# Kernel optimization log

Measured on AMD Instinct MI355X. Metric: run time of the kernel, lower is better.

Reference implementation:

```python
import jax, jax.numpy as jnp
import numpy as np

NUM_NODES = 100000
EMBED_DIM = 64
NUM_LAYERS = 3
NUM_EDGES = 3200000


def setup_inputs() -> dict:
    key = jax.random.key(0)
    k1, k2 = jax.random.split(key)
    # xavier_uniform for [N, D]: bound = sqrt(6/(N+D))
    bound = float(np.sqrt(6.0 / (NUM_NODES + EMBED_DIM)))
    emb = jax.random.uniform(k1, (NUM_NODES, EMBED_DIM), dtype=jnp.float32,
                             minval=-bound, maxval=bound)
    edge_index = jax.random.randint(k2, (2, NUM_EDGES), 0, NUM_NODES, dtype=jnp.int64)
    return {"emb": emb, "edge_index": edge_index}


def reference(emb, edge_index):
    # LightGCN: xs = [x0, LGConv(x0), LGConv^2(x0), ...]; output = mean(xs)
    # LGConv (PyG, add_self_loops=False): out[i] = sum_{(j,i) in E} x[j] / sqrt(d_j * d_i)
    n = emb.shape[0]
    row, col = edge_index[0], edge_index[1]  # row = source j, col = target i
    ones = jnp.ones(row.shape[0], dtype=emb.dtype)
    deg = jax.ops.segment_sum(ones, col, num_segments=n)  # in-degree per gcn_norm
    dinv = jnp.where(deg > 0, jax.lax.rsqrt(jnp.where(deg > 0, deg, 1.0)), 0.0)
    norm = dinv[row] * dinv[col]  # [E]

    x = emb
    acc = emb
    for _ in range(NUM_LAYERS):
        msgs = x[row] * norm[:, None]                      # gather + normalize [E, D]
        x = jax.ops.segment_sum(msgs, col, num_segments=n)  # scatter-add [N, D]
        acc = acc + x
    return acc / (NUM_LAYERS + 1)
```

## Files before the change

kernel.cpp:

```cpp
#include <hip/hip_runtime.h>
#include <hip/hip_bf16.h>
#include <stdint.h>


#define N_NODES 100000
#define N_EDGES 3200000
#define DIM 64

#define NB 196
#define BSH 9
#define BNODES 512
#define CAP 20480

#define CHUNK 8192
#define NBLK1 ((N_EDGES + CHUNK - 1) / CHUNK)

__device__ __forceinline__ float bl(unsigned u) { return __uint_as_float(u << 16); }
__device__ __forceinline__ float bh(unsigned u) { return __uint_as_float(u & 0xffff0000u); }

__global__ __launch_bounds__(256) void k_bucket(const int* __restrict__ ei,
                                                int* __restrict__ gcursor,
                                                int* __restrict__ staging) {
    __shared__ int stage[CHUNK];
    __shared__ unsigned char sbkt[CHUNK];
    __shared__ int bcnt[NB];
    __shared__ int boff[NB];
    __shared__ int bstart[NB];
    __shared__ int gbase[NB];
    __shared__ int wt[4];

    int t = threadIdx.x;
    int e0 = blockIdx.x * CHUNK;
    int nblk = min(CHUNK, N_EDGES - e0);
    int nvec = nblk >> 2;

    const int4* col4 = (const int4*)(ei + N_EDGES + e0);
    const int4* row4 = (const int4*)(ei + e0);

    for (int i = t; i < NB; i += 256) { bcnt[i] = 0; boff[i] = 0; }
    __syncthreads();

    for (int i = t; i < nvec; i += 256) {
        int4 c = col4[i];
        atomicAdd(&bcnt[c.x >> BSH], 1);
        atomicAdd(&bcnt[c.y >> BSH], 1);
        atomicAdd(&bcnt[c.z >> BSH], 1);
        atomicAdd(&bcnt[c.w >> BSH], 1);
    }
    __syncthreads();

    {
        int v = (t < NB) ? bcnt[t] : 0;
        int lane = t & 63, w = t >> 6;
        int s = v;
#pragma unroll
        for (int off = 1; off < 64; off <<= 1) {
            int u = __shfl_up(s, off);
            if (lane >= off) s += u;
        }
        if (lane == 63) wt[w] = s;
        __syncthreads();
        int wo = 0;
        for (int ww = 0; ww < w; ww++) wo += wt[ww];
        if (t < NB) {
            bstart[t] = s - v + wo;
            gbase[t] = (v > 0) ? atomicAdd(&gcursor[t], v) : 0;
        }
    }
    __syncthreads();

    for (int i = t; i < nvec; i += 256) {
        int4 c = col4[i];
        int4 r = row4[i];
        int b0 = c.x >> BSH, b1 = c.y >> BSH, b2 = c.z >> BSH, b3 = c.w >> BSH;
        int p0 = bstart[b0] + atomicAdd(&boff[b0], 1);
        int p1 = bstart[b1] + atomicAdd(&boff[b1], 1);
        int p2 = bstart[b2] + atomicAdd(&boff[b2], 1);
        int p3 = bstart[b3] + atomicAdd(&boff[b3], 1);
        stage[p0] = (r.x << BSH) | (c.x & (BNODES - 1)); sbkt[p0] = (unsigned char)b0;
        stage[p1] = (r.y << BSH) | (c.y & (BNODES - 1)); sbkt[p1] = (unsigned char)b1;
        stage[p2] = (r.z << BSH) | (c.z & (BNODES - 1)); sbkt[p2] = (unsigned char)b2;
        stage[p3] = (r.w << BSH) | (c.w & (BNODES - 1)); sbkt[p3] = (unsigned char)b3;
    }
    __syncthreads();

    for (int i = t; i < nblk; i += 256) {
        int e = stage[i];
        int b = sbkt[i];
        staging[(size_t)b * CAP + gbase[b] + (i - bstart[b])] = e;
    }
}

__global__ void k_bstart(const int* __restrict__ gcursor, int* __restrict__ bucketStart) {
    __shared__ int wt[4];
    int t = threadIdx.x;
    int v = (t < NB) ? gcursor[t] : 0;
    int lane = t & 63, w = t >> 6;
    int s = v;
#pragma unroll
    for (int off = 1; off < 64; off <<= 1) {
        int u = __shfl_up(s, off);
        if (lane >= off) s += u;
    }
    if (lane == 63) wt[w] = s;
    __syncthreads();
    int wo = 0;
    for (int ww = 0; ww < w; ww++) wo += wt[ww];
    if (t < NB) bucketStart[t] = s - v + wo;
}

__global__ __launch_bounds__(256) void k_build(const int* __restrict__ gcursor,
                                               const int* __restrict__ bucketStart,
                                               const int* __restrict__ staging,
                                               int* __restrict__ deg,
                                               int* __restrict__ base,
                                               float* __restrict__ dinv,
                                               int* __restrict__ csrc) {
    __shared__ int ldeg[BNODES];
    __shared__ int lcur[BNODES];
    __shared__ int wt[4];

    int b = blockIdx.x;
    int t = threadIdx.x;
    int n0 = b << BSH;
    int nloc = min(BNODES, N_NODES - n0);
    int cnt = gcursor[b];
    const int* st = staging + (size_t)b * CAP;

    ldeg[t] = 0; ldeg[t + 256] = 0;
    __syncthreads();

    for (int i = t; i < cnt; i += 256) {
        atomicAdd(&ldeg[st[i] & (BNODES - 1)], 1);
    }
    __syncthreads();

    int a0 = ldeg[2 * t], a1 = ldeg[2 * t + 1];
    int s = a0 + a1;
    int lane = t & 63, w = t >> 6;
    int ss = s;
#pragma unroll
    for (int off = 1; off < 64; off <<= 1) {
        int u = __shfl_up(ss, off);
        if (lane >= off) ss += u;
    }
    if (lane == 63) wt[w] = ss;
    __syncthreads();
    int wo = 0;
    for (int ww = 0; ww < w; ww++) wo += wt[ww];
    int excl = ss - s + wo;

    int gb = bucketStart[b] + excl;
    int n = n0 + 2 * t;
    lcur[2 * t] = gb;
    lcur[2 * t + 1] = gb + a0;
    if (2 * t < nloc) {
        deg[n] = a0;
        base[n] = gb;
        dinv[n] = (a0 > 0) ? rsqrtf((float)a0) : 0.0f;
    }
    if (2 * t + 1 < nloc) {
        deg[n + 1] = a1;
        base[n + 1] = gb + a0;
        dinv[n + 1] = (a1 > 0) ? rsqrtf((float)a1) : 0.0f;
    }
    __syncthreads();

    for (int i = t; i < cnt; i += 256) {
        int e = st[i];
        int p = atomicAdd(&lcur[e & (BNODES - 1)], 1);
        csrc[p] = e >> BSH;
    }
}

__global__ void k_z0(const float* __restrict__ emb, const float* __restrict__ dinv,
                     __hip_bfloat16* __restrict__ z) {
    int i = blockIdx.x * blockDim.x + threadIdx.x;
    if (i >= (N_NODES * DIM) / 4) return;
    float di = dinv[(i * 4) >> 6];
    const float4 v = ((const float4*)emb)[i];
    union { ushort h[4]; uint2 u; } pk;
    __hip_bfloat16 b0 = __float2bfloat16(v.x * di);
    __hip_bfloat16 b1 = __float2bfloat16(v.y * di);
    __hip_bfloat16 b2 = __float2bfloat16(v.z * di);
    __hip_bfloat16 b3 = __float2bfloat16(v.w * di);
    pk.h[0] = *(ushort*)&b0; pk.h[1] = *(ushort*)&b1;
    pk.h[2] = *(ushort*)&b2; pk.h[3] = *(ushort*)&b3;
    ((uint2*)z)[i] = pk.u;
}

__global__ __launch_bounds__(256) void k_spmv(
    const int* __restrict__ base, const int* __restrict__ deg,
    const int* __restrict__ csrc, const __hip_bfloat16* __restrict__ z,
    const float* __restrict__ dinv, __hip_bfloat16* __restrict__ znext,
    const float* __restrict__ emb, float* __restrict__ acc_out, int mode) {
    int wave = (blockIdx.x * blockDim.x + threadIdx.x) >> 6;
    int lane = threadIdx.x & 63;
    if (wave >= N_NODES) return;
    int g = lane >> 3;
    int l = lane & 7;

    int start = base[wave];
    int cnt = deg[wave];
    int last = start + max(cnt - 1, 0);

    float acc[8] = {0, 0, 0, 0, 0, 0, 0, 0};

#define ACCUM(U)                                   \
    do {                                           \
        acc[0] += bl((U).x); acc[1] += bh((U).x);  \
        acc[2] += bl((U).y); acc[3] += bh((U).y);  \
        acc[4] += bl((U).z); acc[5] += bh((U).z);  \
        acc[6] += bl((U).w); acc[7] += bh((U).w);  \
    } while (0)

    for (int pos = 0; pos < cnt; pos += 32) {
        int e = pos + g;
        int i0 = start + e;
        int j0 = min(i0, last);
        int j1 = min(i0 + 8, last);
        int j2 = min(i0 + 16, last);
        int j3 = min(i0 + 24, last);
        int s0 = csrc[j0];
        int s1 = csrc[j1];
        int s2 = csrc[j2];
        int s3 = csrc[j3];
        if (e >= cnt)      s0 = N_NODES;
        if (e + 8 >= cnt)  s1 = N_NODES;
        if (e + 16 >= cnt) s2 = N_NODES;
        if (e + 24 >= cnt) s3 = N_NODES;
        uint4 v0 = *((const uint4*)(z + ((size_t)s0 << 6)) + l);
        uint4 v1 = *((const uint4*)(z + ((size_t)s1 << 6)) + l);
        uint4 v2 = *((const uint4*)(z + ((size_t)s2 << 6)) + l);
        uint4 v3 = *((const uint4*)(z + ((size_t)s3 << 6)) + l);
        ACCUM(v0); ACCUM(v1); ACCUM(v2); ACCUM(v3);
    }
#undef ACCUM

#pragma unroll
    for (int j = 0; j < 8; j++) {
        acc[j] += __shfl_xor(acc[j], 8);
        acc[j] += __shfl_xor(acc[j], 16);
        acc[j] += __shfl_xor(acc[j], 32);
    }

    if (lane < 8) {
        float di = dinv[wave];
        size_t o = (size_t)wave * DIM + lane * 8;
        float xo[8];
#pragma unroll
        for (int j = 0; j < 8; j++) xo[j] = acc[j] * di;

        float4 o0, o1;
        if (mode == 0) {
            float4 e0 = ((const float4*)(emb + o))[0];
            float4 e1 = ((const float4*)(emb + o))[1];
            o0 = make_float4(e0.x + xo[0], e0.y + xo[1], e0.z + xo[2], e0.w + xo[3]);
            o1 = make_float4(e1.x + xo[4], e1.y + xo[5], e1.z + xo[6], e1.w + xo[7]);
        } else if (mode == 1) {
            float4 a0 = ((const float4*)(acc_out + o))[0];
            float4 a1 = ((const float4*)(acc_out + o))[1];
            o0 = make_float4(a0.x + xo[0], a0.y + xo[1], a0.z + xo[2], a0.w + xo[3]);
            o1 = make_float4(a1.x + xo[4], a1.y + xo[5], a1.z + xo[6], a1.w + xo[7]);
        } else {
            float4 a0 = ((const float4*)(acc_out + o))[0];
            float4 a1 = ((const float4*)(acc_out + o))[1];
            o0 = make_float4((a0.x + xo[0]) * 0.25f, (a0.y + xo[1]) * 0.25f,
                             (a0.z + xo[2]) * 0.25f, (a0.w + xo[3]) * 0.25f);
            o1 = make_float4((a1.x + xo[4]) * 0.25f, (a1.y + xo[5]) * 0.25f,
                             (a1.z + xo[6]) * 0.25f, (a1.w + xo[7]) * 0.25f);
        }
        ((float4*)(acc_out + o))[0] = o0;
        ((float4*)(acc_out + o))[1] = o1;

        if (mode != 2) {
            union { ushort h[8]; uint4 u; } pk;
#pragma unroll
            for (int j = 0; j < 8; j++) {
                __hip_bfloat16 b = __float2bfloat16(xo[j] * di);
                pk.h[j] = *(ushort*)&b;
            }
            *((uint4*)(znext + o)) = pk.u;
        }
    }
}

extern "C" void kernel_launch(void* const* d_in, const int* in_sizes, int n_in,
                              void* d_out, int out_size, void* d_ws, size_t ws_size,
                              hipStream_t stream) {
    const float* emb = (const float*)d_in[0];
    const int* ei = (const int*)d_in[1];
    float* out = (float*)d_out;

    char* ws = (char*)d_ws;
    size_t off = 0;
    auto alloc = [&](size_t bytes) -> void* {
        void* p = ws + off;
        off += (bytes + 511) & ~(size_t)511;
        return p;
    };
    int* deg = (int*)alloc((size_t)N_NODES * 4);
    float* dinv = (float*)alloc((size_t)N_NODES * 4);
    int* base = (int*)alloc((size_t)N_NODES * 4);
    int* gcursor = (int*)alloc(NB * 4);
    int* bucketStart = (int*)alloc(NB * 4);
    int* csrc = (int*)alloc((size_t)N_EDGES * 4);
    size_t zbytes = (size_t)(N_NODES + 1) * DIM * 2;
    size_t stbytes = (size_t)NB * CAP * 4;
    char* transient = (char*)alloc(stbytes > zbytes ? stbytes : zbytes);
    int* staging = (int*)transient;
    __hip_bfloat16* zA = (__hip_bfloat16*)transient;
    __hip_bfloat16* zB = (__hip_bfloat16*)alloc(zbytes);

    hipMemsetAsync(gcursor, 0, NB * 4, stream);

    k_bucket<<<NBLK1, 256, 0, stream>>>(ei, gcursor, staging);
    k_bstart<<<1, 256, 0, stream>>>(gcursor, bucketStart);
    k_build<<<NB, 256, 0, stream>>>(gcursor, bucketStart, staging, deg, base, dinv, csrc);
    k_z0<<<(N_NODES * DIM / 4 + 255) / 256, 256, 0, stream>>>(emb, dinv, zA);
    hipMemsetAsync(zA + (size_t)N_NODES * DIM, 0, DIM * 2, stream);
    hipMemsetAsync(zB + (size_t)N_NODES * DIM, 0, DIM * 2, stream);

    int spmvBlocks = (N_NODES + 3) / 4;
    k_spmv<<<spmvBlocks, 256, 0, stream>>>(base, deg, csrc, zA, dinv, zB, emb, out, 0);
    k_spmv<<<spmvBlocks, 256, 0, stream>>>(base, deg, csrc, zB, dinv, zA, emb, out, 1);
    k_spmv<<<spmvBlocks, 256, 0, stream>>>(base, deg, csrc, zA, dinv, zB, emb, out, 2);
}
```

Before: 337.7 us.

## Switch gathered features to fp16 with packed half2 accumulation and fold memsets

The normalized feature tables are stored as fp16 instead of bf16, and the SpMV gather now accumulates with packed half2 adds instead of eight fp32 accumulators. Neighbor loads use an exact group count with a remainder path instead of clamped indices. The two sentinel-row memsets are folded into the z0 kernel, and the bucketing chunk size is halved. Accumulating in fp16 reduces ALU work and register use, but it risks precision loss and overflow on sums over high-degree nodes.

```diff
diff --git a/kernel.cpp b/kernel.cpp
--- a/kernel.cpp
+++ b/kernel.cpp
@@ -1,5 +1,6 @@
 #include <hip/hip_runtime.h>
 #include <hip/hip_bf16.h>
+#include <hip/hip_fp16.h>
 #include <stdint.h>
 
 
@@ -12,11 +13,8 @@
 #define BNODES 512
 #define CAP 20480
 
-#define CHUNK 8192
+#define CHUNK 4096
 #define NBLK1 ((N_EDGES + CHUNK - 1) / CHUNK)
-
-__device__ __forceinline__ float bl(unsigned u) { return __uint_as_float(u << 16); }
-__device__ __forceinline__ float bh(unsigned u) { return __uint_as_float(u & 0xffff0000u); }
 
 __global__ __launch_bounds__(256) void k_bucket(const int* __restrict__ ei,
                                                 int* __restrict__ gcursor,
@@ -174,25 +172,31 @@
 }
 
 __global__ void k_z0(const float* __restrict__ emb, const float* __restrict__ dinv,
-                     __hip_bfloat16* __restrict__ z) {
+                     __half* __restrict__ zA, __half* __restrict__ zB) {
+    const int total = (N_NODES * DIM) / 4;
     int i = blockIdx.x * blockDim.x + threadIdx.x;
-    if (i >= (N_NODES * DIM) / 4) return;
+    if (i >= total) {
+        int r = i - total;
+        if (r < 16) ((uint2*)(zA + (size_t)N_NODES * DIM))[r] = make_uint2(0, 0);
+        else if (r < 32) ((uint2*)(zB + (size_t)N_NODES * DIM))[r - 16] = make_uint2(0, 0);
+        return;
+    }
     float di = dinv[(i * 4) >> 6];
     const float4 v = ((const float4*)emb)[i];
     union { ushort h[4]; uint2 u; } pk;
-    __hip_bfloat16 b0 = __float2bfloat16(v.x * di);
-    __hip_bfloat16 b1 = __float2bfloat16(v.y * di);
-    __hip_bfloat16 b2 = __float2bfloat16(v.z * di);
-    __hip_bfloat16 b3 = __float2bfloat16(v.w * di);
-    pk.h[0] = *(ushort*)&b0; pk.h[1] = *(ushort*)&b1;
-    pk.h[2] = *(ushort*)&b2; pk.h[3] = *(ushort*)&b3;
-    ((uint2*)z)[i] = pk.u;
+    __half h0 = __float2half(v.x * di);
+    __half h1 = __float2half(v.y * di);
+    __half h2 = __float2half(v.z * di);
+    __half h3 = __float2half(v.w * di);
+    pk.h[0] = *(ushort*)&h0; pk.h[1] = *(ushort*)&h1;
+    pk.h[2] = *(ushort*)&h2; pk.h[3] = *(ushort*)&h3;
+    ((uint2*)zA)[i] = pk.u;
 }
 
 __global__ __launch_bounds__(256) void k_spmv(
     const int* __restrict__ base, const int* __restrict__ deg,
-    const int* __restrict__ csrc, const __hip_bfloat16* __restrict__ z,
-    const float* __restrict__ dinv, __hip_bfloat16* __restrict__ znext,
+    const int* __restrict__ csrc, const __half* __restrict__ z,
+    const float* __restrict__ dinv, __half* __restrict__ znext,
     const float* __restrict__ emb, float* __restrict__ acc_out, int mode) {
     int wave = (blockIdx.x * blockDim.x + threadIdx.x) >> 6;
     int lane = threadIdx.x & 63;
@@ -202,54 +206,62 @@
 
     int start = base[wave];
     int cnt = deg[wave];
-    int last = start + max(cnt - 1, 0);
-
-    float acc[8] = {0, 0, 0, 0, 0, 0, 0, 0};
-
-#define ACCUM(U)                                   \
-    do {                                           \
-        acc[0] += bl((U).x); acc[1] += bh((U).x);  \
-        acc[2] += bl((U).y); acc[3] += bh((U).y);  \
-        acc[4] += bl((U).z); acc[5] += bh((U).z);  \
-        acc[6] += bl((U).w); acc[7] += bh((U).w);  \
+    float di = dinv[wave];
+    int ng = (cnt + 7) >> 3;
+
+    __half2 hz = __float2half2_rn(0.0f);
+    __half2 hacc0 = hz, hacc1 = hz, hacc2 = hz, hacc3 = hz;
+
+#define GLOAD(KK, SVAR)                              \
+    int e##SVAR = (KK) * 8 + g;                      \
+    int SVAR = csrc[start + e##SVAR];                \
+    SVAR = (e##SVAR < cnt) ? SVAR : N_NODES;
+
+#define GACC(SVAR)                                                        \
+    do {                                                                  \
+        uint4 v = *((const uint4*)(z + ((size_t)SVAR << 6)) + l);         \
+        const __half2* hv = (const __half2*)&v;                           \
+        hacc0 = __hadd2(hacc0, hv[0]);                                    \
+        hacc1 = __hadd2(hacc1, hv[1]);                                    \
+        hacc2 = __hadd2(hacc2, hv[2]);                                    \
+        hacc3 = __hadd2(hacc3, hv[3]);                                    \
     } while (0)
 
-    for (int pos = 0; pos < cnt; pos += 32) {
-        int e = pos + g;
-        int i0 = start + e;
-        int j0 = min(i0, last);
-        int j1 = min(i0 + 8, last);
-        int j2 = min(i0 + 16, last);
-        int j3 = min(i0 + 24, last);
-        int s0 = csrc[j0];
-        int s1 = csrc[j1];
-        int s2 = csrc[j2];
-        int s3 = csrc[j3];
-        if (e >= cnt)      s0 = N_NODES;
-        if (e + 8 >= cnt)  s1 = N_NODES;
-        if (e + 16 >= cnt) s2 = N_NODES;
-        if (e + 24 >= cnt) s3 = N_NODES;
-        uint4 v0 = *((const uint4*)(z + ((size_t)s0 << 6)) + l);
-        uint4 v1 = *((const uint4*)(z + ((size_t)s1 << 6)) + l);
-        uint4 v2 = *((const uint4*)(z + ((size_t)s2 << 6)) + l);
-        uint4 v3 = *((const uint4*)(z + ((size_t)s3 << 6)) + l);
-        ACCUM(v0); ACCUM(v1); ACCUM(v2); ACCUM(v3);
-    }
-#undef ACCUM
-
-#pragma unroll
-    for (int j = 0; j < 8; j++) {
-        acc[j] += __shfl_xor(acc[j], 8);
-        acc[j] += __shfl_xor(acc[j], 16);
-        acc[j] += __shfl_xor(acc[j], 32);
+    int k = 0;
+    for (; k + 4 <= ng; k += 4) {
+        GLOAD(k + 0, s0); GLOAD(k + 1, s1); GLOAD(k + 2, s2); GLOAD(k + 3, s3);
+        GACC(s0); GACC(s1); GACC(s2); GACC(s3);
+    }
+    int rem = ng - k;
+    if (rem > 0) {
+        GLOAD(k + 0, t0);
+        if (rem > 1) { GLOAD(k + 1, t1);
+            if (rem > 2) { GLOAD(k + 2, t2); GACC(t0); GACC(t1); GACC(t2); }
+            else { GACC(t0); GACC(t1); }
+        } else { GACC(t0); }
+    }
+#undef GLOAD
+#undef GACC
+
+#pragma unroll
+    for (int off = 8; off <= 32; off <<= 1) {
+        int b0 = __shfl_xor(*(int*)&hacc0, off);
+        int b1 = __shfl_xor(*(int*)&hacc1, off);
+        int b2 = __shfl_xor(*(int*)&hacc2, off);
+        int b3 = __shfl_xor(*(int*)&hacc3, off);
+        hacc0 = __hadd2(hacc0, *(__half2*)&b0);
+        hacc1 = __hadd2(hacc1, *(__half2*)&b1);
+        hacc2 = __hadd2(hacc2, *(__half2*)&b2);
+        hacc3 = __hadd2(hacc3, *(__half2*)&b3);
     }
 
     if (lane < 8) {
-        float di = dinv[wave];
         size_t o = (size_t)wave * DIM + lane * 8;
         float xo[8];
-#pragma unroll
-        for (int j = 0; j < 8; j++) xo[j] = acc[j] * di;
+        xo[0] = __low2float(hacc0) * di; xo[1] = __high2float(hacc0) * di;
+        xo[2] = __low2float(hacc1) * di; xo[3] = __high2float(hacc1) * di;
+        xo[4] = __low2float(hacc2) * di; xo[5] = __high2float(hacc2) * di;
+        xo[6] = __low2float(hacc3) * di; xo[7] = __high2float(hacc3) * di;
 
         float4 o0, o1;
         if (mode == 0) {
@@ -277,8 +289,8 @@
             union { ushort h[8]; uint4 u; } pk;
 #pragma unroll
             for (int j = 0; j < 8; j++) {
-                __hip_bfloat16 b = __float2bfloat16(xo[j] * di);
-                pk.h[j] = *(ushort*)&b;
+                __half hh = __float2half(xo[j] * di);
+                pk.h[j] = *(ushort*)&hh;
             }
             *((uint4*)(znext + o)) = pk.u;
         }
@@ -304,22 +316,20 @@
     int* base = (int*)alloc((size_t)N_NODES * 4);
     int* gcursor = (int*)alloc(NB * 4);
     int* bucketStart = (int*)alloc(NB * 4);
-    int* csrc = (int*)alloc((size_t)N_EDGES * 4);
+    int* csrc = (int*)alloc(((size_t)N_EDGES + 64) * 4);
     size_t zbytes = (size_t)(N_NODES + 1) * DIM * 2;
     size_t stbytes = (size_t)NB * CAP * 4;
     char* transient = (char*)alloc(stbytes > zbytes ? stbytes : zbytes);
     int* staging = (int*)transient;
-    __hip_bfloat16* zA = (__hip_bfloat16*)transient;
-    __hip_bfloat16* zB = (__hip_bfloat16*)alloc(zbytes);
+    __half* zA = (__half*)transient;
+    __half* zB = (__half*)alloc(zbytes);
 
     hipMemsetAsync(gcursor, 0, NB * 4, stream);
 
     k_bucket<<<NBLK1, 256, 0, stream>>>(ei, gcursor, staging);
     k_bstart<<<1, 256, 0, stream>>>(gcursor, bucketStart);
     k_build<<<NB, 256, 0, stream>>>(gcursor, bucketStart, staging, deg, base, dinv, csrc);
-    k_z0<<<(N_NODES * DIM / 4 + 255) / 256, 256, 0, stream>>>(emb, dinv, zA);
-    hipMemsetAsync(zA + (size_t)N_NODES * DIM, 0, DIM * 2, stream);
-    hipMemsetAsync(zB + (size_t)N_NODES * DIM, 0, DIM * 2, stream);
+    k_z0<<<(N_NODES * DIM / 4) / 256 + 1, 256, 0, stream>>>(emb, dinv, zA, zB);
 
     int spmvBlocks = (N_NODES + 3) / 4;
     k_spmv<<<spmvBlocks, 256, 0, stream>>>(base, deg, csrc, zA, dinv, zB, emb, out, 0);
```

New measurement: 324.7 us. 3.8% less time.
